# Kernel tuning notes

Measured on AMD Instinct MI355X. Metric: run time of the kernel, lower is better.

The kernel has to match this reference:

```python
import jax, jax.numpy as jnp
import numpy as np

S, H, F = 8192, 1024, 15
IN = 1 + F  # scalar target + features per timestep


def _uniform(key, shape, k):
    return jax.random.uniform(key, shape, jnp.float32, -k, k)


def setup_inputs() -> dict:
    key = jax.random.key(0)
    ks = jax.random.split(key, 16)
    k_lstm = 1.0 / np.sqrt(H)  # torch nn.LSTM init scale
    k_ffn = 1.0 / np.sqrt(H)
    return {
        "x": jax.random.normal(ks[0], (S,), jnp.float32),
        "mask": jax.random.randint(ks[1], (S,), 0, 2, jnp.int32),
        "features": jax.random.normal(ks[2], (S, F), jnp.float32),
        "teacher_force_ratio": 1,
        "w_ih0": _uniform(ks[3], (4 * H, IN), k_lstm),
        "w_hh0": _uniform(ks[4], (4 * H, H), k_lstm),
        "b_ih0": _uniform(ks[5], (4 * H,), k_lstm),
        "b_hh0": _uniform(ks[6], (4 * H,), k_lstm),
        "w_ih1": _uniform(ks[7], (4 * H, H), k_lstm),
        "w_hh1": _uniform(ks[8], (4 * H, H), k_lstm),
        "b_ih1": _uniform(ks[9], (4 * H,), k_lstm),
        "b_hh1": _uniform(ks[10], (4 * H,), k_lstm),
        "w_ffn": _uniform(ks[11], (1, H), k_ffn),
        "b_ffn": _uniform(ks[12], (1,), k_ffn),
    }


def _lstm_cell(h, c, inp, w_ih, w_hh, b_ih, b_hh):
    # torch gate order: i, f, g, o
    g = inp @ w_ih.T + h @ w_hh.T + b_ih + b_hh  # (4H,)
    i, f, gg, o = jnp.split(g, 4)
    c_new = jax.nn.sigmoid(f) * c + jax.nn.sigmoid(i) * jnp.tanh(gg)
    h_new = jax.nn.sigmoid(o) * jnp.tanh(c_new)
    return h_new, c_new


def reference(x, mask, features, teacher_force_ratio,
              w_ih0, w_hh0, b_ih0, b_hh0,
              w_ih1, w_hh1, b_ih1, b_hh1,
              w_ffn, b_ffn):
    # teacher_force_ratio==1 => feed x[i] whenever mask[i]!=0 (deterministic).
    # Step 0 always feeds x[0].
    tf = jnp.float32(teacher_force_ratio >= 1)
    use_x = jnp.concatenate([jnp.ones((1,), bool),
                             (mask[1:] != 0) & (tf > 0)])

    def step(carry, inputs):
        h0, c0, h1, c1, prev_y = carry
        xi, sel, fi = inputs
        scalar_in = jnp.where(sel, xi, prev_y)
        inp = jnp.concatenate([scalar_in[None], fi])  # (IN,)
        h0, c0 = _lstm_cell(h0, c0, inp, w_ih0, w_hh0, b_ih0, b_hh0)
        h1, c1 = _lstm_cell(h1, c1, h0, w_ih1, w_hh1, b_ih1, b_hh1)
        y = w_ffn[0] @ h1 + b_ffn[0]  # scalar prediction
        return (h0, c0, h1, c1, y), y

    z = jnp.zeros((H,), x.dtype)
    carry0 = (z, z, z, z, jnp.float32(0.0))
    _, y_hat = jax.lax.scan(step, carry0, (x, use_x, features))
    return y_hat  # (S,)
```

## Files before the change

### kernel.cpp

```cpp
#include <hip/hip_runtime.h>
#include <stdint.h>

typedef float f32x4 __attribute__((ext_vector_type(4)));

#define SLEN 8192
#define NBLK 256

#define RING_PAR 8192
#define H0_OFF   16384
#define MB_OFF   32768
#define MB_STRIDE 32768
#define WS_BYTES (MB_OFF + 8 * MB_STRIDE)

static __device__ __forceinline__ void st_chunk(void* addr, f32x4 v) {
  asm volatile("global_store_dwordx4 %0, %1, off sc0 sc1"
               :: "v"(addr), "v"(v) : "memory");
}
static __device__ __forceinline__ void ld32(const void* a, f32x4& v0, f32x4& v1) {
  asm volatile("global_load_dwordx4 %0, %2, off sc0 sc1\n\t"
               "global_load_dwordx4 %1, %2, off offset:16 sc0 sc1\n\t"
               "s_waitcnt vmcnt(0)"
               : "=v"(v0), "=v"(v1) : "v"(a) : "memory");
}
static __device__ __forceinline__ void poll32(const void* a, unsigned tag,
                                              f32x4& v0, f32x4& v1) {
  ld32(a, v0, v1);
  while (__float_as_uint(v0.w) != tag || __float_as_uint(v1.w) != tag) {
    __builtin_amdgcn_s_sleep(2);
    ld32(a, v0, v1);
  }
}
static __device__ __forceinline__ void ld32_mb(const void* a, f32x4& v0, f32x4& v1) {
  asm volatile("global_load_dwordx4 %0, %2, off sc0\n\t"
               "global_load_dwordx4 %1, %2, off offset:16 sc0\n\t"
               "s_waitcnt vmcnt(0)"
               : "=v"(v0), "=v"(v1) : "v"(a) : "memory");
}
static __device__ __forceinline__ void st_mb(void* a, f32x4 v0, f32x4 v1) {
  asm volatile("global_store_dwordx4 %0, %1, off sc0\n\t"
               "global_store_dwordx4 %0, %2, off offset:16 sc0"
               :: "v"(a), "v"(v0), "v"(v1) : "memory");
}
static __device__ __forceinline__ void poll_rly(const void* mb, const void* ic,
                                                unsigned tag, f32x4& v0, f32x4& v1,
                                                int& dead) {
  if (dead < 4) {
    ld32_mb(mb, v0, v1);
    int tries = 0;
    while (__float_as_uint(v0.w) != tag || __float_as_uint(v1.w) != tag) {
      if (++tries >= 32) break;
      __builtin_amdgcn_s_sleep(1);
      ld32_mb(mb, v0, v1);
    }
    if (__float_as_uint(v0.w) == tag && __float_as_uint(v1.w) == tag) {
      dead = 0;
      return;
    }
    ++dead;
  }
  poll32(ic, tag, v0, v1);
}
static __device__ __forceinline__ void ld_y4(const char* a0, const char* a1,
                                             f32x4& v0, f32x4& v1, f32x4& v2, f32x4& v3) {
  asm volatile("global_load_dwordx4 %0, %4, off sc0 sc1\n\t"
               "global_load_dwordx4 %1, %4, off offset:2048 sc0 sc1\n\t"
               "global_load_dwordx4 %2, %5, off sc0 sc1\n\t"
               "global_load_dwordx4 %3, %5, off offset:2048 sc0 sc1\n\t"
               "s_waitcnt vmcnt(0)"
               : "=v"(v0), "=v"(v1), "=v"(v2), "=v"(v3)
               : "v"(a0), "v"(a1) : "memory");
}
static __device__ __forceinline__ float poll_y4(const char* base, int lane, unsigned tag) {
  const char* a0 = base + lane * 32 + 16;
  const char* a1 = a0 + 4096;
  f32x4 v0, v1, v2, v3;
  ld_y4(a0, a1, v0, v1, v2, v3);
  while (__float_as_uint(v0.w) != tag || __float_as_uint(v1.w) != tag ||
         __float_as_uint(v2.w) != tag || __float_as_uint(v3.w) != tag) {
    __builtin_amdgcn_s_sleep(2);
    ld_y4(a0, a1, v0, v1, v2, v3);
  }
  return (v0.y + v1.y) + (v2.y + v3.y);
}

static __device__ __forceinline__ float sigm(float v) { return 1.f / (1.f + expf(-v)); }
static __device__ __forceinline__ float tanh_f(float v) {
  float e = expf(-2.f * fabsf(v));
  return copysignf((1.f - e) / (1.f + e), v);
}
static __device__ __forceinline__ float lstm_h(float a0, float a1, float a2, float a3,
                                               float& c) {
  float ii = sigm(a0), ff = sigm(a1), gg = tanh_f(a2), oo = sigm(a3);
  c = ff * c + ii * gg;
  return oo * tanh_f(c);
}
static __device__ __forceinline__ float dpp_red(float x) {
  x += __int_as_float(__builtin_amdgcn_update_dpp(0, __float_as_int(x), 0x111, 0xf, 0xf, true));
  x += __int_as_float(__builtin_amdgcn_update_dpp(0, __float_as_int(x), 0x112, 0xf, 0xf, true));
  x += __int_as_float(__builtin_amdgcn_update_dpp(0, __float_as_int(x), 0x114, 0xf, 0xf, true));
  x += __int_as_float(__builtin_amdgcn_update_dpp(0, __float_as_int(x), 0x118, 0xf, 0xf, true));
  x += __int_as_float(__builtin_amdgcn_update_dpp(0, __float_as_int(x), 0x142, 0xa, 0xf, true));
  x += __int_as_float(__builtin_amdgcn_update_dpp(0, __float_as_int(x), 0x143, 0xc, 0xf, true));
  return x;
}
static __device__ __forceinline__ float dot4(f32x4 a, f32x4 b) {
  return a.x * b.x + a.y * b.y + a.z * b.z + a.w * b.w;
}
static __device__ __forceinline__ int lds_idx4(int j) { return (j >> 2) * 20 + (j & 3) * 4; }

__global__ __launch_bounds__(512, 2) void lstm_fused(
    const float* __restrict__ x, const int* __restrict__ mask,
    const float* __restrict__ feat, const int* __restrict__ tfp,
    const float* __restrict__ w_ih0, const float* __restrict__ w_hh0,
    const float* __restrict__ b_ih0, const float* __restrict__ b_hh0,
    const float* __restrict__ w_ih1, const float* __restrict__ w_hh1,
    const float* __restrict__ b_ih1, const float* __restrict__ b_hh1,
    const float* __restrict__ w_ffn, const float* __restrict__ b_ffn,
    float* __restrict__ out, char* __restrict__ ws)
{
  char* h1ring = ws;
  char* h0ring = ws + H0_OFF;
  const int tid = threadIdx.x, lane = tid & 63, wv = tid >> 6;
  const int blk = blockIdx.x;
  const int u = wv & 3;
  const int m = blk * 4 + u;
  const bool L1w = wv < 4;
  const bool leader = blk < 8;
  char* mbx = ws + MB_OFF + (blk & 7) * MB_STRIDE;

  __shared__ __align__(16) float wh1_lds[16 * 1280];
  __shared__ __align__(16) float lh0[1280];
  __shared__ __align__(16) float lh1[1280];
  __shared__ __align__(16) float lyp[256];
  __shared__ float g1h[4], g1yp[4], g0h[4];
  __shared__ float lys;

  f32x4 W[4][4];
  {
    const float* Wsrc = L1w ? w_ih1 : w_hh0;
#pragma unroll
    for (int g = 0; g < 4; ++g) {
      const f32x4* s = reinterpret_cast<const f32x4*>(
          Wsrc + (size_t)(1024 * g + m) * 1024 + lane * 16);
#pragma unroll
      for (int q = 0; q < 4; ++q) W[g][q] = s[q];
    }
  }
  float wA[4], wB[4];
#pragma unroll
  for (int g = 0; g < 4; ++g) {
    const int r = 1024 * g + m;
    if (L1w) {
      wA[g] = (lane == 16) ? (b_ih1[r] + b_hh1[r]) : 0.f;
      wB[g] = 0.f;
    } else {
      wA[g] = (lane < 16) ? w_ih0[r * 16 + lane]
            : (lane == 16 ? (b_ih0[r] + b_hh0[r]) : 0.f);
      wB[g] = w_ih0[r * 16];
    }
  }
  const float wffn_m = w_ffn[m];
  const f32x4 wffn4 = L1w ? reinterpret_cast<const f32x4*>(w_ffn)[tid & 255]
                          : f32x4{0.f, 0.f, 0.f, 0.f};
  const float bf = b_ffn[0];
  float cc = 0.f;
  int fb0 = 0, fb1 = 0;

  for (int ch = tid; ch < 1024; ch += 512) {
    const int r = ch >> 6, kc = ch & 63;
    const int grow = 1024 * (r & 3) + blk * 4 + (r >> 2);
    const f32x4* src = reinterpret_cast<const f32x4*>(
        w_hh1 + (size_t)grow * 1024 + kc * 16);
    f32x4* dst = reinterpret_cast<f32x4*>(&wh1_lds[r * 1280 + kc * 20]);
    dst[0] = src[0]; dst[1] = src[1]; dst[2] = src[2]; dst[3] = src[3];
  }
  __syncthreads();

  const bool tf1 = (*tfp) >= 1;
  float acc0[4];

  for (int t = 0; t < SLEN; ++t) {
    const bool use_x = (t == 0) || (tf1 && mask[t] != 0);
    const bool needy = (t > 0) && !use_x;

    if (L1w) {
      if (t > 0) {
        __builtin_amdgcn_s_setprio(1);
        float a[4];
        const f32x4* h0v = reinterpret_cast<const f32x4*>(&lh0[lane * 20]);
        f32x4 p0 = h0v[0], p1 = h0v[1], p2 = h0v[2], p3 = h0v[3];
#pragma unroll
        for (int g = 0; g < 4; ++g)
          a[g] = wA[g] + dot4(W[g][0], p0) + dot4(W[g][1], p1) +
                          dot4(W[g][2], p2) + dot4(W[g][3], p3);
        if (t > 1) {
          const f32x4* h1v = reinterpret_cast<const f32x4*>(&lh1[lane * 20]);
          f32x4 q0 = h1v[0], q1 = h1v[1], q2 = h1v[2], q3 = h1v[3];
#pragma unroll
          for (int g = 0; g < 4; ++g) {
            const f32x4* wb = reinterpret_cast<const f32x4*>(
                &wh1_lds[(u * 4 + g) * 1280 + lane * 20]);
            a[g] += dot4(wb[0], q0) + dot4(wb[1], q1) +
                    dot4(wb[2], q2) + dot4(wb[3], q3);
          }
        }
#pragma unroll
        for (int g = 0; g < 4; ++g) a[g] = dpp_red(a[g]);
        if (lane == 63) {
          float h = lstm_h(a[0], a[1], a[2], a[3], cc);
          g1h[u] = h; g1yp[u] = wffn_m * h;
        }
        __builtin_amdgcn_s_setprio(0);
      }
    } else {
      float base = (lane == 0) ? (use_x ? x[t] : 0.f)
                 : (lane < 16) ? feat[t * 15 + lane - 1]
                 : (lane == 16) ? 1.f : 0.f;
#pragma unroll
      for (int g = 0; g < 4; ++g) acc0[g] = wA[g] * base;
      if (t > 0) {
        const f32x4* h0v = reinterpret_cast<const f32x4*>(&lh0[lane * 20]);
        f32x4 p0 = h0v[0], p1 = h0v[1], p2 = h0v[2], p3 = h0v[3];
#pragma unroll
        for (int g = 0; g < 4; ++g)
          acc0[g] += dot4(W[g][0], p0) + dot4(W[g][1], p1) +
                     dot4(W[g][2], p2) + dot4(W[g][3], p3);
      }
#pragma unroll
      for (int g = 0; g < 4; ++g) acc0[g] = dpp_red(acc0[g]);
      if (blk == 0 && wv == 7 && t >= 2 && (tf1 && mask[t - 1] != 0)) {
        f32x4 q = reinterpret_cast<const f32x4*>(lyp)[lane];
        float s = (q.x + q.y) + (q.z + q.w);
        s = dpp_red(s);
        if (lane == 63) out[t - 2] = s + bf;
      }
    }
    __syncthreads();

    if (t > 0 && tid < 2) {
      f32x4 v;
      if (tid == 0) { v.x = g1h[0]; v.y = g1h[1]; v.z = g1h[2]; }
      else { v.x = g1h[3]; v.y = (g1yp[0] + g1yp[1]) + (g1yp[2] + g1yp[3]); v.z = 0.f; }
      v.w = __uint_as_float((unsigned)(t - 1));
      st_chunk(h1ring + ((t - 1) & 1) * RING_PAR + blk * 32 + tid * 16, v);
    }

    if (L1w && t > 0 && needy) {
      const char* ic = h1ring + ((t - 1) & 1) * RING_PAR + tid * 32;
      char* mb = mbx + ((t - 1) & 1) * 16384 + tid * 32;
      f32x4 v0, v1;
      if (leader) { poll32(ic, (unsigned)(t - 1), v0, v1); st_mb(mb, v0, v1); }
      else        { poll_rly(mb, ic, (unsigned)(t - 1), v0, v1, fb1); }
      f32x4 h4; h4.x = v0.x; h4.y = v0.y; h4.z = v0.z; h4.w = v1.x;
      *reinterpret_cast<f32x4*>(&lh1[lds_idx4(tid)]) = h4;
      lyp[tid] = dot4(wffn4, h4);
    }
    if (needy) {
      __syncthreads();
      if (wv == 0) {
        f32x4 q = reinterpret_cast<const f32x4*>(lyp)[lane];
        float s = (q.x + q.y) + (q.z + q.w);
        s = dpp_red(s);
        if (lane == 63) {
          float yy = s + bf;
          lys = yy;
          if (blk == 0) out[t - 1] = yy;
        }
      }
      __syncthreads();
    }
    if (!L1w && lane == 63) {
      __builtin_amdgcn_s_setprio(1);
      if (needy) {
        float yy = lys;
#pragma unroll
        for (int g = 0; g < 4; ++g) acc0[g] += yy * wB[g];
      }
      float h = lstm_h(acc0[0], acc0[1], acc0[2], acc0[3], cc);
      g0h[u] = h;
      __builtin_amdgcn_s_setprio(0);
    }
    __syncthreads();

    if (tid < 2) {
      f32x4 v;
      if (tid == 0) { v.x = g0h[0]; v.y = g0h[1]; v.z = g0h[2]; }
      else { v.x = g0h[3]; v.y = 0.f; v.z = 0.f; }
      v.w = __uint_as_float((unsigned)t);
      st_chunk(h0ring + (t & 1) * RING_PAR + blk * 32 + tid * 16, v);
    }

    if (L1w) {
      if (t > 0 && !needy) {
        const char* ic = h1ring + ((t - 1) & 1) * RING_PAR + tid * 32;
        char* mb = mbx + ((t - 1) & 1) * 16384 + tid * 32;
        f32x4 v0, v1;
        if (leader) { poll32(ic, (unsigned)(t - 1), v0, v1); st_mb(mb, v0, v1); }
        else        { poll_rly(mb, ic, (unsigned)(t - 1), v0, v1, fb1); }
        f32x4 h4; h4.x = v0.x; h4.y = v0.y; h4.z = v0.z; h4.w = v1.x;
        *reinterpret_cast<f32x4*>(&lh1[lds_idx4(tid)]) = h4;
        lyp[tid] = dot4(wffn4, h4);
      }
    } else {
      const int j = tid - 256;
      const char* ic = h0ring + (t & 1) * RING_PAR + j * 32;
      char* mb = mbx + (t & 1) * 16384 + 8192 + j * 32;
      f32x4 v0, v1;
      if (leader) { poll32(ic, (unsigned)t, v0, v1); st_mb(mb, v0, v1); }
      else        { poll_rly(mb, ic, (unsigned)t, v0, v1, fb0); }
      f32x4 h4; h4.x = v0.x; h4.y = v0.y; h4.z = v0.z; h4.w = v1.x;
      *reinterpret_cast<f32x4*>(&lh0[lds_idx4(j)]) = h4;
    }
    __syncthreads();
  }

  if (L1w) {
    float a[4];
    const f32x4* h0v = reinterpret_cast<const f32x4*>(&lh0[lane * 20]);
    f32x4 p0 = h0v[0], p1 = h0v[1], p2 = h0v[2], p3 = h0v[3];
#pragma unroll
    for (int g = 0; g < 4; ++g)
      a[g] = wA[g] + dot4(W[g][0], p0) + dot4(W[g][1], p1) +
                      dot4(W[g][2], p2) + dot4(W[g][3], p3);
    {
      const f32x4* h1v = reinterpret_cast<const f32x4*>(&lh1[lane * 20]);
      f32x4 q0 = h1v[0], q1 = h1v[1], q2 = h1v[2], q3 = h1v[3];
#pragma unroll
      for (int g = 0; g < 4; ++g) {
        const f32x4* wb = reinterpret_cast<const f32x4*>(
            &wh1_lds[(u * 4 + g) * 1280 + lane * 20]);
        a[g] += dot4(wb[0], q0) + dot4(wb[1], q1) +
                dot4(wb[2], q2) + dot4(wb[3], q3);
      }
    }
#pragma unroll
    for (int g = 0; g < 4; ++g) a[g] = dpp_red(a[g]);
    if (lane == 63) {
      float h = lstm_h(a[0], a[1], a[2], a[3], cc);
      g1h[u] = h; g1yp[u] = wffn_m * h;
    }
  } else if (blk == 0 && wv == 7 && (tf1 && mask[SLEN - 1] != 0)) {
    f32x4 q = reinterpret_cast<const f32x4*>(lyp)[lane];
    float s = (q.x + q.y) + (q.z + q.w);
    s = dpp_red(s);
    if (lane == 63) out[SLEN - 2] = s + bf;
  }
  __syncthreads();
  if (tid < 2) {
    f32x4 v;
    if (tid == 0) { v.x = g1h[0]; v.y = g1h[1]; v.z = g1h[2]; }
    else { v.x = g1h[3]; v.y = (g1yp[0] + g1yp[1]) + (g1yp[2] + g1yp[3]); v.z = 0.f; }
    v.w = __uint_as_float((unsigned)(SLEN - 1));
    st_chunk(h1ring + ((SLEN - 1) & 1) * RING_PAR + blk * 32 + tid * 16, v);
  }
  if (blk == 0 && wv == 0) {
    float s = poll_y4(h1ring + ((SLEN - 1) & 1) * RING_PAR, lane, (unsigned)(SLEN - 1));
    s = dpp_red(s);
    if (lane == 63) out[SLEN - 1] = s + bf;
  }
}

extern "C" void kernel_launch(void* const* d_in, const int* in_sizes, int n_in,
                              void* d_out, int out_size, void* d_ws, size_t ws_size,
                              hipStream_t stream) {
  (void)in_sizes; (void)n_in; (void)out_size; (void)ws_size;
  const float* x      = (const float*)d_in[0];
  const int*   mask   = (const int*)  d_in[1];
  const float* feat   = (const float*)d_in[2];
  const int*   tfp    = (const int*)  d_in[3];
  const float* w_ih0  = (const float*)d_in[4];
  const float* w_hh0  = (const float*)d_in[5];
  const float* b_ih0  = (const float*)d_in[6];
  const float* b_hh0  = (const float*)d_in[7];
  const float* w_ih1  = (const float*)d_in[8];
  const float* w_hh1  = (const float*)d_in[9];
  const float* b_ih1  = (const float*)d_in[10];
  const float* b_hh1  = (const float*)d_in[11];
  const float* w_ffn  = (const float*)d_in[12];
  const float* b_ffn  = (const float*)d_in[13];
  float* out = (float*)d_out;
  char*  ws  = (char*)d_ws;

  hipMemsetAsync(d_ws, 0xFF, (size_t)WS_BYTES, stream);

  lstm_fused<<<dim3(NBLK), dim3(512), 0, stream>>>(
      x, mask, feat, tfp, w_ih0, w_hh0, b_ih0, b_hh0,
      w_ih1, w_hh1, b_ih1, b_hh1, w_ffn, b_ffn, out, ws);
}
```

Baseline: 38.83 ms.

## Compute feedback y per layer-0 wave via direct polling, drop extra barriers

On steps that feed back the previous prediction, the layer-0 waves now each poll the h1 ring (through the mailbox relay when possible) for the partial y sums and reduce them themselves. This replaces the path where L1 waves loaded h1, wave 0 reduced, and the result went through LDS between two extra block barriers. Leader blocks also drop the sleep in their global polls to react faster. The cost is more redundant polling traffic and busier spinning on the interconnect.

```diff
diff --git a/kernel.cpp b/kernel.cpp
--- a/kernel.cpp
+++ b/kernel.cpp
@@ -27,6 +27,13 @@
   ld32(a, v0, v1);
   while (__float_as_uint(v0.w) != tag || __float_as_uint(v1.w) != tag) {
     __builtin_amdgcn_s_sleep(2);
+    ld32(a, v0, v1);
+  }
+}
+static __device__ __forceinline__ void poll32_ns(const void* a, unsigned tag,
+                                                 f32x4& v0, f32x4& v1) {
+  ld32(a, v0, v1);
+  while (__float_as_uint(v0.w) != tag || __float_as_uint(v1.w) != tag) {
     ld32(a, v0, v1);
   }
 }
@@ -60,8 +67,18 @@
   }
   poll32(ic, tag, v0, v1);
 }
-static __device__ __forceinline__ void ld_y4(const char* a0, const char* a1,
-                                             f32x4& v0, f32x4& v1, f32x4& v2, f32x4& v3) {
+static __device__ __forceinline__ void ld_y4_mb(const char* a0, const char* a1,
+                                                f32x4& v0, f32x4& v1, f32x4& v2, f32x4& v3) {
+  asm volatile("global_load_dwordx4 %0, %4, off sc0\n\t"
+               "global_load_dwordx4 %1, %4, off offset:2048 sc0\n\t"
+               "global_load_dwordx4 %2, %5, off sc0\n\t"
+               "global_load_dwordx4 %3, %5, off offset:2048 sc0\n\t"
+               "s_waitcnt vmcnt(0)"
+               : "=v"(v0), "=v"(v1), "=v"(v2), "=v"(v3)
+               : "v"(a0), "v"(a1) : "memory");
+}
+static __device__ __forceinline__ void ld_y4_ic(const char* a0, const char* a1,
+                                                f32x4& v0, f32x4& v1, f32x4& v2, f32x4& v3) {
   asm volatile("global_load_dwordx4 %0, %4, off sc0 sc1\n\t"
                "global_load_dwordx4 %1, %4, off offset:2048 sc0 sc1\n\t"
                "global_load_dwordx4 %2, %5, off sc0 sc1\n\t"
@@ -70,15 +87,36 @@
                : "=v"(v0), "=v"(v1), "=v"(v2), "=v"(v3)
                : "v"(a0), "v"(a1) : "memory");
 }
-static __device__ __forceinline__ float poll_y4(const char* base, int lane, unsigned tag) {
-  const char* a0 = base + lane * 32 + 16;
+static __device__ __forceinline__ bool y4_ok(f32x4 v0, f32x4 v1, f32x4 v2, f32x4 v3,
+                                             unsigned tag) {
+  return __float_as_uint(v0.w) == tag && __float_as_uint(v1.w) == tag &&
+         __float_as_uint(v2.w) == tag && __float_as_uint(v3.w) == tag;
+}
+static __device__ __forceinline__ float poll_y4(const char* mb_base, const char* ic_base,
+                                                int lane, unsigned tag, int& dead) {
+  f32x4 v0, v1, v2, v3;
+  if (dead < 4) {
+    const char* a0 = mb_base + lane * 32 + 16;
+    const char* a1 = a0 + 4096;
+    ld_y4_mb(a0, a1, v0, v1, v2, v3);
+    int tries = 0;
+    while (!y4_ok(v0, v1, v2, v3, tag)) {
+      if (++tries >= 32) break;
+      __builtin_amdgcn_s_sleep(1);
+      ld_y4_mb(a0, a1, v0, v1, v2, v3);
+    }
+    if (y4_ok(v0, v1, v2, v3, tag)) {
+      dead = 0;
+      return (v0.y + v1.y) + (v2.y + v3.y);
+    }
+    ++dead;
+  }
+  const char* a0 = ic_base + lane * 32 + 16;
   const char* a1 = a0 + 4096;
-  f32x4 v0, v1, v2, v3;
-  ld_y4(a0, a1, v0, v1, v2, v3);
-  while (__float_as_uint(v0.w) != tag || __float_as_uint(v1.w) != tag ||
-         __float_as_uint(v2.w) != tag || __float_as_uint(v3.w) != tag) {
+  ld_y4_ic(a0, a1, v0, v1, v2, v3);
+  while (!y4_ok(v0, v1, v2, v3, tag)) {
     __builtin_amdgcn_s_sleep(2);
-    ld_y4(a0, a1, v0, v1, v2, v3);
+    ld_y4_ic(a0, a1, v0, v1, v2, v3);
   }
   return (v0.y + v1.y) + (v2.y + v3.y);
 }
@@ -133,7 +171,6 @@
   __shared__ __align__(16) float lh1[1280];
   __shared__ __align__(16) float lyp[256];
   __shared__ float g1h[4], g1yp[4], g0h[4];
-  __shared__ float lys;
 
   f32x4 W[4][4];
   {
@@ -164,7 +201,7 @@
                           : f32x4{0.f, 0.f, 0.f, 0.f};
   const float bf = b_ffn[0];
   float cc = 0.f;
-  int fb0 = 0, fb1 = 0;
+  int fb0 = 0, fb1 = 0, fby = 0;
 
   for (int ch = tid; ch < 1024; ch += 512) {
     const int r = ch >> 6, kc = ch & 63;
@@ -245,37 +282,31 @@
       st_chunk(h1ring + ((t - 1) & 1) * RING_PAR + blk * 32 + tid * 16, v);
     }
 
-    if (L1w && t > 0 && needy) {
-      const char* ic = h1ring + ((t - 1) & 1) * RING_PAR + tid * 32;
-      char* mb = mbx + ((t - 1) & 1) * 16384 + tid * 32;
-      f32x4 v0, v1;
-      if (leader) { poll32(ic, (unsigned)(t - 1), v0, v1); st_mb(mb, v0, v1); }
-      else        { poll_rly(mb, ic, (unsigned)(t - 1), v0, v1, fb1); }
-      f32x4 h4; h4.x = v0.x; h4.y = v0.y; h4.z = v0.z; h4.w = v1.x;
-      *reinterpret_cast<f32x4*>(&lh1[lds_idx4(tid)]) = h4;
-      lyp[tid] = dot4(wffn4, h4);
-    }
     if (needy) {
-      __syncthreads();
-      if (wv == 0) {
-        f32x4 q = reinterpret_cast<const f32x4*>(lyp)[lane];
-        float s = (q.x + q.y) + (q.z + q.w);
+      if (L1w) {
+        const char* ic = h1ring + ((t - 1) & 1) * RING_PAR + tid * 32;
+        char* mb = mbx + ((t - 1) & 1) * 16384 + tid * 32;
+        f32x4 v0, v1;
+        if (leader) { poll32_ns(ic, (unsigned)(t - 1), v0, v1); st_mb(mb, v0, v1); }
+        else        { poll_rly(mb, ic, (unsigned)(t - 1), v0, v1, fb1); }
+        f32x4 h4; h4.x = v0.x; h4.y = v0.y; h4.z = v0.z; h4.w = v1.x;
+        *reinterpret_cast<f32x4*>(&lh1[lds_idx4(tid)]) = h4;
+        lyp[tid] = dot4(wffn4, h4);
+      } else {
+        float s = poll_y4(mbx + ((t - 1) & 1) * 16384,
+                          h1ring + ((t - 1) & 1) * RING_PAR, lane,
+                          (unsigned)(t - 1), fby);
         s = dpp_red(s);
         if (lane == 63) {
           float yy = s + bf;
-          lys = yy;
-          if (blk == 0) out[t - 1] = yy;
+          if (blk == 0 && wv == 4) out[t - 1] = yy;
+#pragma unroll
+          for (int g = 0; g < 4; ++g) acc0[g] += yy * wB[g];
         }
       }
-      __syncthreads();
     }
     if (!L1w && lane == 63) {
       __builtin_amdgcn_s_setprio(1);
-      if (needy) {
-        float yy = lys;
-#pragma unroll
-        for (int g = 0; g < 4; ++g) acc0[g] += yy * wB[g];
-      }
       float h = lstm_h(acc0[0], acc0[1], acc0[2], acc0[3], cc);
       g0h[u] = h;
       __builtin_amdgcn_s_setprio(0);
@@ -295,7 +326,7 @@
         const char* ic = h1ring + ((t - 1) & 1) * RING_PAR + tid * 32;
         char* mb = mbx + ((t - 1) & 1) * 16384 + tid * 32;
         f32x4 v0, v1;
-        if (leader) { poll32(ic, (unsigned)(t - 1), v0, v1); st_mb(mb, v0, v1); }
+        if (leader) { poll32_ns(ic, (unsigned)(t - 1), v0, v1); st_mb(mb, v0, v1); }
         else        { poll_rly(mb, ic, (unsigned)(t - 1), v0, v1, fb1); }
         f32x4 h4; h4.x = v0.x; h4.y = v0.y; h4.z = v0.z; h4.w = v1.x;
         *reinterpret_cast<f32x4*>(&lh1[lds_idx4(tid)]) = h4;
@@ -306,7 +337,7 @@
       const char* ic = h0ring + (t & 1) * RING_PAR + j * 32;
       char* mb = mbx + (t & 1) * 16384 + 8192 + j * 32;
       f32x4 v0, v1;
-      if (leader) { poll32(ic, (unsigned)t, v0, v1); st_mb(mb, v0, v1); }
+      if (leader) { poll32_ns(ic, (unsigned)t, v0, v1); st_mb(mb, v0, v1); }
       else        { poll_rly(mb, ic, (unsigned)t, v0, v1, fb0); }
       f32x4 h4; h4.x = v0.x; h4.y = v0.y; h4.z = v0.z; h4.w = v1.x;
       *reinterpret_cast<f32x4*>(&lh0[lds_idx4(j)]) = h4;
@@ -354,7 +385,10 @@
     st_chunk(h1ring + ((SLEN - 1) & 1) * RING_PAR + blk * 32 + tid * 16, v);
   }
   if (blk == 0 && wv == 0) {
-    float s = poll_y4(h1ring + ((SLEN - 1) & 1) * RING_PAR, lane, (unsigned)(SLEN - 1));
+    int dead = 4;
+    float s = poll_y4(mbx + ((SLEN - 1) & 1) * 16384,
+                      h1ring + ((SLEN - 1) & 1) * RING_PAR, lane,
+                      (unsigned)(SLEN - 1), dead);
     s = dpp_red(s);
     if (lane == 63) out[SLEN - 1] = s + bf;
   }
```

After: 40.82 ms. +5.1%, slower.

## Replace per-step block barriers with LDS flag handoffs and double-buffered hidden state

Applied to the files above, without the earlier changes.

Each timestep used to pass through several __syncthreads barriers. These are replaced with workgroup-scope acquire/release flags in LDS, so individual waves can publish layer-0 and layer-1 hidden values and the FFN partials as soon as they are ready. The h0/h1 LDS buffers and the y-partials become double-buffered so one step can overlap the next, leaving only one barrier per step. The spin-polls also drop their s_sleep calls, which cuts wake-up latency but raises memory-polling traffic, and the spin-wait protocol adds ordering and deadlock risk.

```diff
diff --git a/kernel.cpp b/kernel.cpp
--- a/kernel.cpp
+++ b/kernel.cpp
@@ -12,6 +12,9 @@
 #define MB_STRIDE 32768
 #define WS_BYTES (MB_OFF + 8 * MB_STRIDE)
 
+#define LDS_REL(p, v) __hip_atomic_store((p), (v), __ATOMIC_RELEASE, __HIP_MEMORY_SCOPE_WORKGROUP)
+#define LDS_ACQ(p)    __hip_atomic_load((p), __ATOMIC_ACQUIRE, __HIP_MEMORY_SCOPE_WORKGROUP)
+
 static __device__ __forceinline__ void st_chunk(void* addr, f32x4 v) {
   asm volatile("global_store_dwordx4 %0, %1, off sc0 sc1"
                :: "v"(addr), "v"(v) : "memory");
@@ -27,6 +30,13 @@
   ld32(a, v0, v1);
   while (__float_as_uint(v0.w) != tag || __float_as_uint(v1.w) != tag) {
     __builtin_amdgcn_s_sleep(2);
+    ld32(a, v0, v1);
+  }
+}
+static __device__ __forceinline__ void poll32_ns(const void* a, unsigned tag,
+                                                 f32x4& v0, f32x4& v1) {
+  ld32(a, v0, v1);
+  while (__float_as_uint(v0.w) != tag || __float_as_uint(v1.w) != tag) {
     ld32(a, v0, v1);
   }
 }
@@ -48,8 +58,7 @@
     ld32_mb(mb, v0, v1);
     int tries = 0;
     while (__float_as_uint(v0.w) != tag || __float_as_uint(v1.w) != tag) {
-      if (++tries >= 32) break;
-      __builtin_amdgcn_s_sleep(1);
+      if (++tries >= 64) break;
       ld32_mb(mb, v0, v1);
     }
     if (__float_as_uint(v0.w) == tag && __float_as_uint(v1.w) == tag) {
@@ -59,28 +68,6 @@
     ++dead;
   }
   poll32(ic, tag, v0, v1);
-}
-static __device__ __forceinline__ void ld_y4(const char* a0, const char* a1,
-                                             f32x4& v0, f32x4& v1, f32x4& v2, f32x4& v3) {
-  asm volatile("global_load_dwordx4 %0, %4, off sc0 sc1\n\t"
-               "global_load_dwordx4 %1, %4, off offset:2048 sc0 sc1\n\t"
-               "global_load_dwordx4 %2, %5, off sc0 sc1\n\t"
-               "global_load_dwordx4 %3, %5, off offset:2048 sc0 sc1\n\t"
-               "s_waitcnt vmcnt(0)"
-               : "=v"(v0), "=v"(v1), "=v"(v2), "=v"(v3)
-               : "v"(a0), "v"(a1) : "memory");
-}
-static __device__ __forceinline__ float poll_y4(const char* base, int lane, unsigned tag) {
-  const char* a0 = base + lane * 32 + 16;
-  const char* a1 = a0 + 4096;
-  f32x4 v0, v1, v2, v3;
-  ld_y4(a0, a1, v0, v1, v2, v3);
-  while (__float_as_uint(v0.w) != tag || __float_as_uint(v1.w) != tag ||
-         __float_as_uint(v2.w) != tag || __float_as_uint(v3.w) != tag) {
-    __builtin_amdgcn_s_sleep(2);
-    ld_y4(a0, a1, v0, v1, v2, v3);
-  }
-  return (v0.y + v1.y) + (v2.y + v3.y);
 }
 
 static __device__ __forceinline__ float sigm(float v) { return 1.f / (1.f + expf(-v)); }
@@ -129,11 +116,12 @@
   char* mbx = ws + MB_OFF + (blk & 7) * MB_STRIDE;
 
   __shared__ __align__(16) float wh1_lds[16 * 1280];
-  __shared__ __align__(16) float lh0[1280];
-  __shared__ __align__(16) float lh1[1280];
-  __shared__ __align__(16) float lyp[256];
-  __shared__ float g1h[4], g1yp[4], g0h[4];
-  __shared__ float lys;
+  __shared__ __align__(16) float lh0[2][1280];
+  __shared__ __align__(16) float lh1[2][1280];
+  __shared__ float g1hv[4], g0hv[4];
+  __shared__ unsigned g1ht[4], g0ht[4];
+  __shared__ float ypv[2][4];
+  __shared__ unsigned ypt[2][4];
 
   f32x4 W[4][4];
   {
@@ -159,13 +147,16 @@
       wB[g] = w_ih0[r * 16];
     }
   }
-  const float wffn_m = w_ffn[m];
   const f32x4 wffn4 = L1w ? reinterpret_cast<const f32x4*>(w_ffn)[tid & 255]
                           : f32x4{0.f, 0.f, 0.f, 0.f};
   const float bf = b_ffn[0];
   float cc = 0.f;
   int fb0 = 0, fb1 = 0;
 
+  if (tid < 4) {
+    g1ht[tid] = 0xFFFFFFFFu; g0ht[tid] = 0xFFFFFFFFu;
+    ypt[0][tid] = 0xFFFFFFFFu; ypt[1][tid] = 0xFFFFFFFFu;
+  }
   for (int ch = tid; ch < 1024; ch += 512) {
     const int r = ch >> 6, kc = ch & 63;
     const int grow = 1024 * (r & 3) + blk * 4 + (r >> 2);
@@ -187,14 +178,14 @@
       if (t > 0) {
         __builtin_amdgcn_s_setprio(1);
         float a[4];
-        const f32x4* h0v = reinterpret_cast<const f32x4*>(&lh0[lane * 20]);
+        const f32x4* h0v = reinterpret_cast<const f32x4*>(&lh0[(t - 1) & 1][lane * 20]);
         f32x4 p0 = h0v[0], p1 = h0v[1], p2 = h0v[2], p3 = h0v[3];
 #pragma unroll
         for (int g = 0; g < 4; ++g)
           a[g] = wA[g] + dot4(W[g][0], p0) + dot4(W[g][1], p1) +
                           dot4(W[g][2], p2) + dot4(W[g][3], p3);
         if (t > 1) {
-          const f32x4* h1v = reinterpret_cast<const f32x4*>(&lh1[lane * 20]);
+          const f32x4* h1v = reinterpret_cast<const f32x4*>(&lh1[t & 1][lane * 20]);
           f32x4 q0 = h1v[0], q1 = h1v[1], q2 = h1v[2], q3 = h1v[3];
 #pragma unroll
           for (int g = 0; g < 4; ++g) {
@@ -208,18 +199,61 @@
         for (int g = 0; g < 4; ++g) a[g] = dpp_red(a[g]);
         if (lane == 63) {
           float h = lstm_h(a[0], a[1], a[2], a[3], cc);
-          g1h[u] = h; g1yp[u] = wffn_m * h;
+          g1hv[u] = h;
+          LDS_REL(&g1ht[u], (unsigned)(t - 1));
         }
         __builtin_amdgcn_s_setprio(0);
+      }
+      if (blk == 0 && wv == 3 && lane == 0 && t >= 2 && (tf1 && mask[t - 1] != 0)) {
+        const int sl = (t - 2) & 1;
+        out[t - 2] = ((ypv[sl][0] + ypv[sl][1]) + (ypv[sl][2] + ypv[sl][3])) + bf;
+      }
+      const bool fun_first = (wv == 0) && !needy;
+      if (fun_first && lane < 2) {
+        while (LDS_ACQ(&g0ht[0]) != (unsigned)t) {}
+        while (LDS_ACQ(&g0ht[1]) != (unsigned)t) {}
+        while (LDS_ACQ(&g0ht[2]) != (unsigned)t) {}
+        while (LDS_ACQ(&g0ht[3]) != (unsigned)t) {}
+        f32x4 v;
+        if (lane == 0) { v.x = g0hv[0]; v.y = g0hv[1]; v.z = g0hv[2]; }
+        else           { v.x = g0hv[3]; v.y = 0.f; v.z = 0.f; }
+        v.w = __uint_as_float((unsigned)t);
+        st_chunk(h0ring + (t & 1) * RING_PAR + blk * 32 + lane * 16, v);
+      }
+      if (t > 0) {
+        const char* ic = h1ring + ((t - 1) & 1) * RING_PAR + tid * 32;
+        char* mb = mbx + ((t - 1) & 1) * 16384 + tid * 32;
+        f32x4 v0, v1;
+        if (leader) { poll32_ns(ic, (unsigned)(t - 1), v0, v1); st_mb(mb, v0, v1); }
+        else        { poll_rly(mb, ic, (unsigned)(t - 1), v0, v1, fb1); }
+        f32x4 h4; h4.x = v0.x; h4.y = v0.y; h4.z = v0.z; h4.w = v1.x;
+        *reinterpret_cast<f32x4*>(&lh1[(t - 1) & 1][lds_idx4(tid)]) = h4;
+        float p = dpp_red(dot4(wffn4, h4));
+        if (lane == 63) {
+          ypv[(t - 1) & 1][u] = p;
+          LDS_REL(&ypt[(t - 1) & 1][u], (unsigned)(t - 1));
+        }
+      }
+      if (!fun_first && wv == 0 && lane < 2) {
+        while (LDS_ACQ(&g0ht[0]) != (unsigned)t) {}
+        while (LDS_ACQ(&g0ht[1]) != (unsigned)t) {}
+        while (LDS_ACQ(&g0ht[2]) != (unsigned)t) {}
+        while (LDS_ACQ(&g0ht[3]) != (unsigned)t) {}
+        f32x4 v;
+        if (lane == 0) { v.x = g0hv[0]; v.y = g0hv[1]; v.z = g0hv[2]; }
+        else           { v.x = g0hv[3]; v.y = 0.f; v.z = 0.f; }
+        v.w = __uint_as_float((unsigned)t);
+        st_chunk(h0ring + (t & 1) * RING_PAR + blk * 32 + lane * 16, v);
       }
     } else {
       float base = (lane == 0) ? (use_x ? x[t] : 0.f)
                  : (lane < 16) ? feat[t * 15 + lane - 1]
                  : (lane == 16) ? 1.f : 0.f;
+      __builtin_amdgcn_s_setprio(1);
 #pragma unroll
       for (int g = 0; g < 4; ++g) acc0[g] = wA[g] * base;
       if (t > 0) {
-        const f32x4* h0v = reinterpret_cast<const f32x4*>(&lh0[lane * 20]);
+        const f32x4* h0v = reinterpret_cast<const f32x4*>(&lh0[(t - 1) & 1][lane * 20]);
         f32x4 p0 = h0v[0], p1 = h0v[1], p2 = h0v[2], p3 = h0v[3];
 #pragma unroll
         for (int g = 0; g < 4; ++g)
@@ -228,102 +262,60 @@
       }
 #pragma unroll
       for (int g = 0; g < 4; ++g) acc0[g] = dpp_red(acc0[g]);
-      if (blk == 0 && wv == 7 && t >= 2 && (tf1 && mask[t - 1] != 0)) {
-        f32x4 q = reinterpret_cast<const f32x4*>(lyp)[lane];
-        float s = (q.x + q.y) + (q.z + q.w);
-        s = dpp_red(s);
-        if (lane == 63) out[t - 2] = s + bf;
-      }
-    }
-    __syncthreads();
-
-    if (t > 0 && tid < 2) {
-      f32x4 v;
-      if (tid == 0) { v.x = g1h[0]; v.y = g1h[1]; v.z = g1h[2]; }
-      else { v.x = g1h[3]; v.y = (g1yp[0] + g1yp[1]) + (g1yp[2] + g1yp[3]); v.z = 0.f; }
-      v.w = __uint_as_float((unsigned)(t - 1));
-      st_chunk(h1ring + ((t - 1) & 1) * RING_PAR + blk * 32 + tid * 16, v);
-    }
-
-    if (L1w && t > 0 && needy) {
-      const char* ic = h1ring + ((t - 1) & 1) * RING_PAR + tid * 32;
-      char* mb = mbx + ((t - 1) & 1) * 16384 + tid * 32;
-      f32x4 v0, v1;
-      if (leader) { poll32(ic, (unsigned)(t - 1), v0, v1); st_mb(mb, v0, v1); }
-      else        { poll_rly(mb, ic, (unsigned)(t - 1), v0, v1, fb1); }
-      f32x4 h4; h4.x = v0.x; h4.y = v0.y; h4.z = v0.z; h4.w = v1.x;
-      *reinterpret_cast<f32x4*>(&lh1[lds_idx4(tid)]) = h4;
-      lyp[tid] = dot4(wffn4, h4);
-    }
-    if (needy) {
-      __syncthreads();
-      if (wv == 0) {
-        f32x4 q = reinterpret_cast<const f32x4*>(lyp)[lane];
-        float s = (q.x + q.y) + (q.z + q.w);
-        s = dpp_red(s);
-        if (lane == 63) {
-          float yy = s + bf;
-          lys = yy;
-          if (blk == 0) out[t - 1] = yy;
+      __builtin_amdgcn_s_setprio(0);
+      if (wv == 4 && lane < 2 && t > 0) {
+        while (LDS_ACQ(&g1ht[0]) != (unsigned)(t - 1)) {}
+        while (LDS_ACQ(&g1ht[1]) != (unsigned)(t - 1)) {}
+        while (LDS_ACQ(&g1ht[2]) != (unsigned)(t - 1)) {}
+        while (LDS_ACQ(&g1ht[3]) != (unsigned)(t - 1)) {}
+        f32x4 v;
+        if (lane == 0) { v.x = g1hv[0]; v.y = g1hv[1]; v.z = g1hv[2]; }
+        else           { v.x = g1hv[3]; v.y = 0.f; v.z = 0.f; }
+        v.w = __uint_as_float((unsigned)(t - 1));
+        st_chunk(h1ring + ((t - 1) & 1) * RING_PAR + blk * 32 + lane * 16, v);
+      }
+      if (lane == 63) {
+        if (needy) {
+          const int sl = (t - 1) & 1;
+          while (LDS_ACQ(&ypt[sl][0]) != (unsigned)(t - 1)) {}
+          while (LDS_ACQ(&ypt[sl][1]) != (unsigned)(t - 1)) {}
+          while (LDS_ACQ(&ypt[sl][2]) != (unsigned)(t - 1)) {}
+          while (LDS_ACQ(&ypt[sl][3]) != (unsigned)(t - 1)) {}
+          float yy = ((ypv[sl][0] + ypv[sl][1]) + (ypv[sl][2] + ypv[sl][3])) + bf;
+          if (blk == 0 && wv == 4) out[t - 1] = yy;
+#pragma unroll
+          for (int g = 0; g < 4; ++g) acc0[g] += yy * wB[g];
         }
-      }
-      __syncthreads();
-    }
-    if (!L1w && lane == 63) {
-      __builtin_amdgcn_s_setprio(1);
-      if (needy) {
-        float yy = lys;
-#pragma unroll
-        for (int g = 0; g < 4; ++g) acc0[g] += yy * wB[g];
-      }
-      float h = lstm_h(acc0[0], acc0[1], acc0[2], acc0[3], cc);
-      g0h[u] = h;
-      __builtin_amdgcn_s_setprio(0);
-    }
-    __syncthreads();
-
-    if (tid < 2) {
-      f32x4 v;
-      if (tid == 0) { v.x = g0h[0]; v.y = g0h[1]; v.z = g0h[2]; }
-      else { v.x = g0h[3]; v.y = 0.f; v.z = 0.f; }
-      v.w = __uint_as_float((unsigned)t);
-      st_chunk(h0ring + (t & 1) * RING_PAR + blk * 32 + tid * 16, v);
-    }
-
-    if (L1w) {
-      if (t > 0 && !needy) {
-        const char* ic = h1ring + ((t - 1) & 1) * RING_PAR + tid * 32;
-        char* mb = mbx + ((t - 1) & 1) * 16384 + tid * 32;
-        f32x4 v0, v1;
-        if (leader) { poll32(ic, (unsigned)(t - 1), v0, v1); st_mb(mb, v0, v1); }
-        else        { poll_rly(mb, ic, (unsigned)(t - 1), v0, v1, fb1); }
-        f32x4 h4; h4.x = v0.x; h4.y = v0.y; h4.z = v0.z; h4.w = v1.x;
-        *reinterpret_cast<f32x4*>(&lh1[lds_idx4(tid)]) = h4;
-        lyp[tid] = dot4(wffn4, h4);
-      }
-    } else {
+        float h = lstm_h(acc0[0], acc0[1], acc0[2], acc0[3], cc);
+        g0hv[u] = h;
+        LDS_REL(&g0ht[u], (unsigned)t);
+      }
       const int j = tid - 256;
       const char* ic = h0ring + (t & 1) * RING_PAR + j * 32;
       char* mb = mbx + (t & 1) * 16384 + 8192 + j * 32;
       f32x4 v0, v1;
-      if (leader) { poll32(ic, (unsigned)t, v0, v1); st_mb(mb, v0, v1); }
+      if (leader) { poll32_ns(ic, (unsigned)t, v0, v1); st_mb(mb, v0, v1); }
       else        { poll_rly(mb, ic, (unsigned)t, v0, v1, fb0); }
       f32x4 h4; h4.x = v0.x; h4.y = v0.y; h4.z = v0.z; h4.w = v1.x;
-      *reinterpret_cast<f32x4*>(&lh0[lds_idx4(j)]) = h4;
+      *reinterpret_cast<f32x4*>(&lh0[t & 1][lds_idx4(j)]) = h4;
     }
     __syncthreads();
   }
 
+  if (blk == 0 && wv == 3 && lane == 0 && (tf1 && mask[SLEN - 1] != 0)) {
+    const int sl = (SLEN - 2) & 1;
+    out[SLEN - 2] = ((ypv[sl][0] + ypv[sl][1]) + (ypv[sl][2] + ypv[sl][3])) + bf;
+  }
   if (L1w) {
     float a[4];
-    const f32x4* h0v = reinterpret_cast<const f32x4*>(&lh0[lane * 20]);
+    const f32x4* h0v = reinterpret_cast<const f32x4*>(&lh0[(SLEN - 1) & 1][lane * 20]);
     f32x4 p0 = h0v[0], p1 = h0v[1], p2 = h0v[2], p3 = h0v[3];
 #pragma unroll
     for (int g = 0; g < 4; ++g)
       a[g] = wA[g] + dot4(W[g][0], p0) + dot4(W[g][1], p1) +
                       dot4(W[g][2], p2) + dot4(W[g][3], p3);
     {
-      const f32x4* h1v = reinterpret_cast<const f32x4*>(&lh1[lane * 20]);
+      const f32x4* h1v = reinterpret_cast<const f32x4*>(&lh1[(SLEN - 2) & 1][lane * 20]);
       f32x4 q0 = h1v[0], q1 = h1v[1], q2 = h1v[2], q3 = h1v[3];
 #pragma unroll
       for (int g = 0; g < 4; ++g) {
@@ -337,26 +329,38 @@
     for (int g = 0; g < 4; ++g) a[g] = dpp_red(a[g]);
     if (lane == 63) {
       float h = lstm_h(a[0], a[1], a[2], a[3], cc);
-      g1h[u] = h; g1yp[u] = wffn_m * h;
-    }
-  } else if (blk == 0 && wv == 7 && (tf1 && mask[SLEN - 1] != 0)) {
-    f32x4 q = reinterpret_cast<const f32x4*>(lyp)[lane];
-    float s = (q.x + q.y) + (q.z + q.w);
-    s = dpp_red(s);
-    if (lane == 63) out[SLEN - 2] = s + bf;
-  }
-  __syncthreads();
-  if (tid < 2) {
+      g1hv[u] = h;
+      LDS_REL(&g1ht[u], (unsigned)(SLEN - 1));
+    }
+  } else if (wv == 4 && lane < 2) {
+    while (LDS_ACQ(&g1ht[0]) != (unsigned)(SLEN - 1)) {}
+    while (LDS_ACQ(&g1ht[1]) != (unsigned)(SLEN - 1)) {}
+    while (LDS_ACQ(&g1ht[2]) != (unsigned)(SLEN - 1)) {}
+    while (LDS_ACQ(&g1ht[3]) != (unsigned)(SLEN - 1)) {}
     f32x4 v;
-    if (tid == 0) { v.x = g1h[0]; v.y = g1h[1]; v.z = g1h[2]; }
-    else { v.x = g1h[3]; v.y = (g1yp[0] + g1yp[1]) + (g1yp[2] + g1yp[3]); v.z = 0.f; }
+    if (lane == 0) { v.x = g1hv[0]; v.y = g1hv[1]; v.z = g1hv[2]; }
+    else           { v.x = g1hv[3]; v.y = 0.f; v.z = 0.f; }
     v.w = __uint_as_float((unsigned)(SLEN - 1));
-    st_chunk(h1ring + ((SLEN - 1) & 1) * RING_PAR + blk * 32 + tid * 16, v);
-  }
-  if (blk == 0 && wv == 0) {
-    float s = poll_y4(h1ring + ((SLEN - 1) & 1) * RING_PAR, lane, (unsigned)(SLEN - 1));
-    s = dpp_red(s);
-    if (lane == 63) out[SLEN - 1] = s + bf;
+    st_chunk(h1ring + ((SLEN - 1) & 1) * RING_PAR + blk * 32 + lane * 16, v);
+    asm volatile("s_waitcnt vmcnt(0)" ::: "memory");
+  }
+  if (blk == 0 && L1w) {
+    f32x4 v0, v1;
+    poll32(h1ring + ((SLEN - 1) & 1) * RING_PAR + tid * 32, (unsigned)(SLEN - 1), v0, v1);
+    f32x4 h4; h4.x = v0.x; h4.y = v0.y; h4.z = v0.z; h4.w = v1.x;
+    float p = dpp_red(dot4(wffn4, h4));
+    if (lane == 63) {
+      ypv[(SLEN - 1) & 1][u] = p;
+      LDS_REL(&ypt[(SLEN - 1) & 1][u], (unsigned)(SLEN - 1));
+    }
+  }
+  if (blk == 0 && wv == 3 && lane == 1) {
+    const int sl = (SLEN - 1) & 1;
+    while (LDS_ACQ(&ypt[sl][0]) != (unsigned)(SLEN - 1)) {}
+    while (LDS_ACQ(&ypt[sl][1]) != (unsigned)(SLEN - 1)) {}
+    while (LDS_ACQ(&ypt[sl][2]) != (unsigned)(SLEN - 1)) {}
+    while (LDS_ACQ(&ypt[sl][3]) != (unsigned)(SLEN - 1)) {}
+    out[SLEN - 1] = ((ypv[sl][0] + ypv[sl][1]) + (ypv[sl][2] + ypv[sl][3])) + bf;
   }
 }
 
```

Measured after the change: 48.19 ms. 1.24x slower.

## Restructure per-step sync: direct per-wave h0 publish, merged staging, busy-poll without sleep

Applied to the files above, without the earlier changes.

Each layer-0 wave now publishes its own h0 chunk directly to the global ring. This removes the shared g0h buffer, one block barrier and the tid<2 publish stage. Staging of h0 and h1 is split across all L1 waves, with the ring layout widened to 64 bytes per block. The y prediction is reduced per wave with DPP into ypv instead of a separate wave-0 reduction pass. Spin loops drop s_sleep for lower wake latency, at the cost of more memory polling traffic and a risk of ordering or race bugs in the new schedule.

```diff
diff --git a/kernel.cpp b/kernel.cpp
--- a/kernel.cpp
+++ b/kernel.cpp
@@ -6,10 +6,10 @@
 #define SLEN 8192
 #define NBLK 256
 
-#define RING_PAR 8192
-#define H0_OFF   16384
-#define MB_OFF   32768
-#define MB_STRIDE 32768
+#define H0_RING 16384
+#define MB_OFF  49152
+#define MB_STRIDE 49152
+#define MB_H0   16384
 #define WS_BYTES (MB_OFF + 8 * MB_STRIDE)
 
 static __device__ __forceinline__ void st_chunk(void* addr, f32x4 v) {
@@ -27,6 +27,13 @@
   ld32(a, v0, v1);
   while (__float_as_uint(v0.w) != tag || __float_as_uint(v1.w) != tag) {
     __builtin_amdgcn_s_sleep(2);
+    ld32(a, v0, v1);
+  }
+}
+static __device__ __forceinline__ void poll32_ns(const void* a, unsigned tag,
+                                                 f32x4& v0, f32x4& v1) {
+  ld32(a, v0, v1);
+  while (__float_as_uint(v0.w) != tag || __float_as_uint(v1.w) != tag) {
     ld32(a, v0, v1);
   }
 }
@@ -48,8 +55,7 @@
     ld32_mb(mb, v0, v1);
     int tries = 0;
     while (__float_as_uint(v0.w) != tag || __float_as_uint(v1.w) != tag) {
-      if (++tries >= 32) break;
-      __builtin_amdgcn_s_sleep(1);
+      if (++tries >= 64) break;
       ld32_mb(mb, v0, v1);
     }
     if (__float_as_uint(v0.w) == tag && __float_as_uint(v1.w) == tag) {
@@ -59,28 +65,6 @@
     ++dead;
   }
   poll32(ic, tag, v0, v1);
-}
-static __device__ __forceinline__ void ld_y4(const char* a0, const char* a1,
-                                             f32x4& v0, f32x4& v1, f32x4& v2, f32x4& v3) {
-  asm volatile("global_load_dwordx4 %0, %4, off sc0 sc1\n\t"
-               "global_load_dwordx4 %1, %4, off offset:2048 sc0 sc1\n\t"
-               "global_load_dwordx4 %2, %5, off sc0 sc1\n\t"
-               "global_load_dwordx4 %3, %5, off offset:2048 sc0 sc1\n\t"
-               "s_waitcnt vmcnt(0)"
-               : "=v"(v0), "=v"(v1), "=v"(v2), "=v"(v3)
-               : "v"(a0), "v"(a1) : "memory");
-}
-static __device__ __forceinline__ float poll_y4(const char* base, int lane, unsigned tag) {
-  const char* a0 = base + lane * 32 + 16;
-  const char* a1 = a0 + 4096;
-  f32x4 v0, v1, v2, v3;
-  ld_y4(a0, a1, v0, v1, v2, v3);
-  while (__float_as_uint(v0.w) != tag || __float_as_uint(v1.w) != tag ||
-         __float_as_uint(v2.w) != tag || __float_as_uint(v3.w) != tag) {
-    __builtin_amdgcn_s_sleep(2);
-    ld_y4(a0, a1, v0, v1, v2, v3);
-  }
-  return (v0.y + v1.y) + (v2.y + v3.y);
 }
 
 static __device__ __forceinline__ float sigm(float v) { return 1.f / (1.f + expf(-v)); }
@@ -106,7 +90,8 @@
 static __device__ __forceinline__ float dot4(f32x4 a, f32x4 b) {
   return a.x * b.x + a.y * b.y + a.z * b.z + a.w * b.w;
 }
-static __device__ __forceinline__ int lds_idx4(int j) { return (j >> 2) * 20 + (j & 3) * 4; }
+static __device__ __forceinline__ int lidx(int k)   { return (k >> 4) * 20 + (k & 15); }
+static __device__ __forceinline__ int lidx4(int j)  { return (j >> 2) * 20 + (j & 3) * 4; }
 
 __global__ __launch_bounds__(512, 2) void lstm_fused(
     const float* __restrict__ x, const int* __restrict__ mask,
@@ -119,7 +104,7 @@
     float* __restrict__ out, char* __restrict__ ws)
 {
   char* h1ring = ws;
-  char* h0ring = ws + H0_OFF;
+  char* h0ring = ws + H0_RING;
   const int tid = threadIdx.x, lane = tid & 63, wv = tid >> 6;
   const int blk = blockIdx.x;
   const int u = wv & 3;
@@ -131,19 +116,20 @@
   __shared__ __align__(16) float wh1_lds[16 * 1280];
   __shared__ __align__(16) float lh0[1280];
   __shared__ __align__(16) float lh1[1280];
-  __shared__ __align__(16) float lyp[256];
-  __shared__ float g1h[4], g1yp[4], g0h[4];
-  __shared__ float lys;
+  __shared__ float g1h[4], g1yp[4];
+  __shared__ float ypv[2][4];
+  __shared__ float lyp_t[256];
+  __shared__ float part[4];
 
   f32x4 W[4][4];
   {
     const float* Wsrc = L1w ? w_ih1 : w_hh0;
 #pragma unroll
     for (int g = 0; g < 4; ++g) {
-      const f32x4* s = reinterpret_cast<const f32x4*>(
+      const f32x4* sp = reinterpret_cast<const f32x4*>(
           Wsrc + (size_t)(1024 * g + m) * 1024 + lane * 16);
 #pragma unroll
-      for (int q = 0; q < 4; ++q) W[g][q] = s[q];
+      for (int q = 0; q < 4; ++q) W[g][q] = sp[q];
     }
   }
   float wA[4], wB[4];
@@ -179,9 +165,34 @@
   const bool tf1 = (*tfp) >= 1;
   float acc0[4];
 
+  auto stage_h0 = [&](int t) {
+    const unsigned tg = (unsigned)t;
+    const int j = tid >> 1, half = tid & 1;
+    const char* ic = h0ring + (t & 1) * 16384 + j * 64 + half * 32;
+    char* mb = mbx + MB_H0 + (t & 1) * 16384 + j * 64 + half * 32;
+    f32x4 v0, v1;
+    if (leader) { poll32_ns(ic, tg, v0, v1); st_mb(mb, v0, v1); }
+    else        { poll_rly(mb, ic, tg, v0, v1, fb0); }
+    const int b = lidx(j * 4 + half * 2);
+    lh0[b] = v0.x; lh0[b + 1] = v1.x;
+  };
+  auto stage_h1 = [&](int t) {
+    const unsigned tg = (unsigned)(t - 1);
+    const char* ic = h1ring + ((t - 1) & 1) * 8192 + tid * 32;
+    char* mb = mbx + ((t - 1) & 1) * 8192 + tid * 32;
+    f32x4 v0, v1;
+    if (leader) { poll32_ns(ic, tg, v0, v1); st_mb(mb, v0, v1); }
+    else        { poll_rly(mb, ic, tg, v0, v1, fb1); }
+    f32x4 h4; h4.x = v0.x; h4.y = v0.y; h4.z = v0.z; h4.w = v1.x;
+    *reinterpret_cast<f32x4*>(&lh1[lidx4(tid)]) = h4;
+    float p = dpp_red(dot4(wffn4, h4));
+    if (lane == 63) ypv[(t - 1) & 1][u] = p;
+  };
+
   for (int t = 0; t < SLEN; ++t) {
     const bool use_x = (t == 0) || (tf1 && mask[t] != 0);
-    const bool needy = (t > 0) && !use_x;
+    const bool needy = !use_x;
+    const unsigned tg = (unsigned)t;
 
     if (L1w) {
       if (t > 0) {
@@ -213,6 +224,10 @@
         __builtin_amdgcn_s_setprio(0);
       }
     } else {
+      if (blk == 0 && wv == 7 && lane == 0 && t >= 2 && (tf1 && mask[t - 1] != 0)) {
+        const int sl = t & 1;
+        out[t - 2] = ((ypv[sl][0] + ypv[sl][1]) + (ypv[sl][2] + ypv[sl][3])) + bf;
+      }
       float base = (lane == 0) ? (use_x ? x[t] : 0.f)
                  : (lane < 16) ? feat[t * 15 + lane - 1]
                  : (lane == 16) ? 1.f : 0.f;
@@ -228,11 +243,10 @@
       }
 #pragma unroll
       for (int g = 0; g < 4; ++g) acc0[g] = dpp_red(acc0[g]);
-      if (blk == 0 && wv == 7 && t >= 2 && (tf1 && mask[t - 1] != 0)) {
-        f32x4 q = reinterpret_cast<const f32x4*>(lyp)[lane];
-        float s = (q.x + q.y) + (q.z + q.w);
-        s = dpp_red(s);
-        if (lane == 63) out[t - 2] = s + bf;
+      if (use_x && lane == 63) {
+        float h = lstm_h(acc0[0], acc0[1], acc0[2], acc0[3], cc);
+        f32x4 v; v.x = h; v.y = 0.f; v.z = 0.f; v.w = __uint_as_float(tg);
+        st_chunk(h0ring + (t & 1) * 16384 + blk * 64 + u * 16, v);
       }
     }
     __syncthreads();
@@ -242,78 +256,41 @@
       if (tid == 0) { v.x = g1h[0]; v.y = g1h[1]; v.z = g1h[2]; }
       else { v.x = g1h[3]; v.y = (g1yp[0] + g1yp[1]) + (g1yp[2] + g1yp[3]); v.z = 0.f; }
       v.w = __uint_as_float((unsigned)(t - 1));
-      st_chunk(h1ring + ((t - 1) & 1) * RING_PAR + blk * 32 + tid * 16, v);
-    }
-
-    if (L1w && t > 0 && needy) {
-      const char* ic = h1ring + ((t - 1) & 1) * RING_PAR + tid * 32;
-      char* mb = mbx + ((t - 1) & 1) * 16384 + tid * 32;
-      f32x4 v0, v1;
-      if (leader) { poll32(ic, (unsigned)(t - 1), v0, v1); st_mb(mb, v0, v1); }
-      else        { poll_rly(mb, ic, (unsigned)(t - 1), v0, v1, fb1); }
-      f32x4 h4; h4.x = v0.x; h4.y = v0.y; h4.z = v0.z; h4.w = v1.x;
-      *reinterpret_cast<f32x4*>(&lh1[lds_idx4(tid)]) = h4;
-      lyp[tid] = dot4(wffn4, h4);
+      st_chunk(h1ring + ((t - 1) & 1) * 8192 + blk * 32 + tid * 16, v);
+    }
+
+    if (L1w) {
+      if (!needy) {
+        stage_h0(t);
+        if (t > 0) stage_h1(t);
+      } else {
+        stage_h1(t);
+      }
     }
     if (needy) {
       __syncthreads();
-      if (wv == 0) {
-        f32x4 q = reinterpret_cast<const f32x4*>(lyp)[lane];
-        float s = (q.x + q.y) + (q.z + q.w);
-        s = dpp_red(s);
-        if (lane == 63) {
-          float yy = s + bf;
-          lys = yy;
-          if (blk == 0) out[t - 1] = yy;
-        }
-      }
-      __syncthreads();
-    }
-    if (!L1w && lane == 63) {
-      __builtin_amdgcn_s_setprio(1);
-      if (needy) {
-        float yy = lys;
+      if (!L1w && lane == 63) {
+        __builtin_amdgcn_s_setprio(1);
+        const int sl = (t - 1) & 1;
+        float yy = ((ypv[sl][0] + ypv[sl][1]) + (ypv[sl][2] + ypv[sl][3])) + bf;
+        if (blk == 0 && wv == 4) out[t - 1] = yy;
 #pragma unroll
         for (int g = 0; g < 4; ++g) acc0[g] += yy * wB[g];
-      }
-      float h = lstm_h(acc0[0], acc0[1], acc0[2], acc0[3], cc);
-      g0h[u] = h;
-      __builtin_amdgcn_s_setprio(0);
-    }
+        float h = lstm_h(acc0[0], acc0[1], acc0[2], acc0[3], cc);
+        f32x4 v; v.x = h; v.y = 0.f; v.z = 0.f; v.w = __uint_as_float(tg);
+        st_chunk(h0ring + (t & 1) * 16384 + blk * 64 + u * 16, v);
+        __builtin_amdgcn_s_setprio(0);
+      }
+      if (L1w) stage_h0(t);
+    }
+    if (!L1w) stage_h0(t);
     __syncthreads();
-
-    if (tid < 2) {
-      f32x4 v;
-      if (tid == 0) { v.x = g0h[0]; v.y = g0h[1]; v.z = g0h[2]; }
-      else { v.x = g0h[3]; v.y = 0.f; v.z = 0.f; }
-      v.w = __uint_as_float((unsigned)t);
-      st_chunk(h0ring + (t & 1) * RING_PAR + blk * 32 + tid * 16, v);
-    }
-
-    if (L1w) {
-      if (t > 0 && !needy) {
-        const char* ic = h1ring + ((t - 1) & 1) * RING_PAR + tid * 32;
-        char* mb = mbx + ((t - 1) & 1) * 16384 + tid * 32;
-        f32x4 v0, v1;
-        if (leader) { poll32(ic, (unsigned)(t - 1), v0, v1); st_mb(mb, v0, v1); }
-        else        { poll_rly(mb, ic, (unsigned)(t - 1), v0, v1, fb1); }
-        f32x4 h4; h4.x = v0.x; h4.y = v0.y; h4.z = v0.z; h4.w = v1.x;
-        *reinterpret_cast<f32x4*>(&lh1[lds_idx4(tid)]) = h4;
-        lyp[tid] = dot4(wffn4, h4);
-      }
-    } else {
-      const int j = tid - 256;
-      const char* ic = h0ring + (t & 1) * RING_PAR + j * 32;
-      char* mb = mbx + (t & 1) * 16384 + 8192 + j * 32;
-      f32x4 v0, v1;
-      if (leader) { poll32(ic, (unsigned)t, v0, v1); st_mb(mb, v0, v1); }
-      else        { poll_rly(mb, ic, (unsigned)t, v0, v1, fb0); }
-      f32x4 h4; h4.x = v0.x; h4.y = v0.y; h4.z = v0.z; h4.w = v1.x;
-      *reinterpret_cast<f32x4*>(&lh0[lds_idx4(j)]) = h4;
-    }
-    __syncthreads();
-  }
-
+  }
+
+  if (blk == 0 && wv == 7 && lane == 0 && (tf1 && mask[SLEN - 1] != 0)) {
+    const int sl = SLEN & 1;
+    out[SLEN - 2] = ((ypv[sl][0] + ypv[sl][1]) + (ypv[sl][2] + ypv[sl][3])) + bf;
+  }
   if (L1w) {
     float a[4];
     const f32x4* h0v = reinterpret_cast<const f32x4*>(&lh0[lane * 20]);
@@ -339,11 +316,6 @@
       float h = lstm_h(a[0], a[1], a[2], a[3], cc);
       g1h[u] = h; g1yp[u] = wffn_m * h;
     }
-  } else if (blk == 0 && wv == 7 && (tf1 && mask[SLEN - 1] != 0)) {
-    f32x4 q = reinterpret_cast<const f32x4*>(lyp)[lane];
-    float s = (q.x + q.y) + (q.z + q.w);
-    s = dpp_red(s);
-    if (lane == 63) out[SLEN - 2] = s + bf;
   }
   __syncthreads();
   if (tid < 2) {
@@ -351,12 +323,21 @@
     if (tid == 0) { v.x = g1h[0]; v.y = g1h[1]; v.z = g1h[2]; }
     else { v.x = g1h[3]; v.y = (g1yp[0] + g1yp[1]) + (g1yp[2] + g1yp[3]); v.z = 0.f; }
     v.w = __uint_as_float((unsigned)(SLEN - 1));
-    st_chunk(h1ring + ((SLEN - 1) & 1) * RING_PAR + blk * 32 + tid * 16, v);
-  }
-  if (blk == 0 && wv == 0) {
-    float s = poll_y4(h1ring + ((SLEN - 1) & 1) * RING_PAR, lane, (unsigned)(SLEN - 1));
-    s = dpp_red(s);
-    if (lane == 63) out[SLEN - 1] = s + bf;
+    st_chunk(h1ring + ((SLEN - 1) & 1) * 8192 + blk * 32 + tid * 16, v);
+  }
+  if (blk == 0) {
+    if (tid < 256) {
+      f32x4 v0, v1;
+      poll32(h1ring + ((SLEN - 1) & 1) * 8192 + tid * 32, (unsigned)(SLEN - 1), v0, v1);
+      lyp_t[tid] = v1.y;
+    }
+    __syncthreads();
+    if (wv < 4) {
+      float p = dpp_red(lyp_t[wv * 64 + lane]);
+      if (lane == 63) part[wv] = p;
+    }
+    __syncthreads();
+    if (tid == 0) out[SLEN - 1] = ((part[0] + part[1]) + (part[2] + part[3])) + bf;
   }
 }
 
```

Result: slower. 48.60 ms (+25.2%).
